# Optimization experiments

Measured on AMD Instinct MI355X. Metric: run time of the kernel, lower is better.

The kernel has to match this reference:

```python
import jax, jax.numpy as jnp
import numpy as np

B, S, D, H, HH, L = 256, 512, 128, 256, 128, 64
PATH_V, SYS_V = 10000, 500

def _gru_cell(gi_t, h, Whh, bhh):
    # PyTorch GRU cell: gi_t = x @ Wih.T + bih precomputed
    gh = h @ Whh.T + bhh
    ir, iz, inn = jnp.split(gi_t, 3, axis=-1)
    hr, hz, hn = jnp.split(gh, 3, axis=-1)
    r = jax.nn.sigmoid(ir + hr)
    z = jax.nn.sigmoid(iz + hz)
    n = jnp.tanh(inn + r * hn)
    return (1.0 - z) * n + z * h

def _gru_seq(x, Wih, Whh, bih, bhh):
    # x: [B,S,in] -> outputs [B,S,H], zero initial hidden (torch default)
    gi = jnp.einsum('bsd,hd->bsh', x, Wih) + bih  # precompute input gates once
    h0 = jnp.zeros((x.shape[0], Whh.shape[1]), x.dtype)
    def step(h, gi_t):
        hn = _gru_cell(gi_t, h, Whh, bhh)
        return hn, hn
    _, ys = jax.lax.scan(step, h0, jnp.swapaxes(gi, 0, 1))
    return jnp.swapaxes(ys, 0, 1)

def setup_inputs() -> dict:
    key = jax.random.key(0)
    ks = jax.random.split(key, 24)
    r = lambda k, shape: (jax.random.normal(k, shape, dtype=jnp.float32) * 0.05)
    inp = {
        'tokens': jax.random.randint(ks[0], (B, S, 2), 0, SYS_V, dtype=jnp.int64),
        'path_emb_w': r(ks[1], (PATH_V, D)),
        'sys_emb_w': r(ks[2], (SYS_V, D)),
        # encoder gru1: D -> H
        'e1_Wih': r(ks[3], (3 * H, D)), 'e1_Whh': r(ks[4], (3 * H, H)),
        'e1_bih': r(ks[5], (3 * H,)), 'e1_bhh': r(ks[6], (3 * H,)),
        # encoder gru2: H -> HH
        'e2_Wih': r(ks[7], (3 * HH, H)), 'e2_Whh': r(ks[8], (3 * HH, HH)),
        'e2_bih': r(ks[9], (3 * HH,)), 'e2_bhh': r(ks[10], (3 * HH,)),
        # linear1: HH -> L
        'l1_W': r(ks[11], (L, HH)), 'l1_b': r(ks[12], (L,)),
        # decoder gru1: L -> HH
        'd1_Wih': r(ks[13], (3 * HH, L)), 'd1_Whh': r(ks[14], (3 * HH, HH)),
        'd1_bih': r(ks[15], (3 * HH,)), 'd1_bhh': r(ks[16], (3 * HH,)),
        # decoder gru2: HH -> H
        'd2_Wih': r(ks[17], (3 * H, HH)), 'd2_Whh': r(ks[18], (3 * H, H)),
        'd2_bih': r(ks[19], (3 * H,)), 'd2_bhh': r(ks[20], (3 * H,)),
        # linear2: H -> D
        'l2_W': r(ks[21], (D, H)), 'l2_b': r(ks[22], (D,)),
    }
    return inp

def reference(tokens, path_emb_w, sys_emb_w,
              e1_Wih, e1_Whh, e1_bih, e1_bhh,
              e2_Wih, e2_Whh, e2_bih, e2_bhh,
              l1_W, l1_b,
              d1_Wih, d1_Whh, d1_bih, d1_bhh,
              d2_Wih, d2_Whh, d2_bih, d2_bhh,
              l2_W, l2_b):
    # embedding sum -> [B,S,D]
    emb = path_emb_w[tokens[:, :, 0]] + sys_emb_w[tokens[:, :, 1]]
    # encoder (dropout is identity at eval)
    h1_seq = _gru_seq(emb, e1_Wih, e1_Whh, e1_bih, e1_bhh)      # [B,S,H]
    h2_seq = _gru_seq(h1_seq, e2_Wih, e2_Whh, e2_bih, e2_bhh)    # [B,S,HH]
    latent = h2_seq[:, -1, :] @ l1_W.T + l1_b                    # [B,L]
    gi1 = latent @ d1_Wih.T + d1_bih                             # constant [B,3*HH]
    h10 = jnp.zeros((latent.shape[0], HH), latent.dtype)
    h20 = jnp.zeros((latent.shape[0], H), latent.dtype)
    def dec_step(carry, _):
        h1, h2 = carry
        h1 = _gru_cell(gi1, h1, d1_Whh, d1_bhh)
        gi2 = h1 @ d2_Wih.T + d2_bih
        h2 = _gru_cell(gi2, h2, d2_Whh, d2_bhh)
        out = h2 @ l2_W.T + l2_b                                 # linear2 per step
        return (h1, h2), out
    _, outs = jax.lax.scan(dec_step, (h10, h20), None, length=S)  # [S,B,D]
    recon = jnp.swapaxes(outs, 0, 1)                             # [B,S,D]
    recon_loss = jnp.mean((recon - emb) ** 2)
    return latent, recon_loss
```

## Files before the change

kernel.cpp:

```cpp
#include <hip/hip_runtime.h>
#include <cstddef>

typedef unsigned short u16;
typedef __bf16 bf16x8 __attribute__((ext_vector_type(8)));
typedef float f32x4 __attribute__((ext_vector_type(4)));
typedef unsigned short us4 __attribute__((ext_vector_type(4)));

__device__ __forceinline__ u16 f2b(float f) {
    unsigned u = __float_as_uint(f);
    u += 0x7fffu + ((u >> 16) & 1u);
    return (u16)(u >> 16);
}
__device__ __forceinline__ float b2f(u16 h) { return __uint_as_float(((unsigned)h) << 16); }

__device__ __forceinline__ f32x4 mfma16(bf16x8 a, bf16x8 b, f32x4 c) {
    return __builtin_amdgcn_mfma_f32_16x16x32_bf16(a, b, c, 0, 0, 0);
}

__device__ __forceinline__ void bar_lds() {
    asm volatile("s_waitcnt lgkmcnt(0)\n\ts_barrier" ::: "memory");
}

#define CH   64
#define NCH  8
#define MCH  (CH * 256)

struct PackSeg { const float* src; u16* dst; int K; int nfrag; };
struct PackArgs { PackSeg seg[8]; };

__global__ __launch_bounds__(64) void pack_all(PackArgs pa) {
    int f = blockIdx.x;
    int i = 0;
    while (i < 7 && f >= pa.seg[i].nfrag) { f -= pa.seg[i].nfrag; i++; }
    const float* W = pa.seg[i].src;
    u16* out = pa.seg[i].dst;
    int K = pa.seg[i].K;
    int lane = threadIdx.x, q = lane >> 4, ln = lane & 15;
    int KT = K >> 5;
    int nt = f / KT, kt = f % KT;
    int n = nt * 16 + ln;
    int kb = kt * 32 + q * 8;
#pragma unroll
    for (int j = 0; j < 8; j++)
        out[((size_t)f * 64 + lane) * 8 + j] = f2b(W[(size_t)n * K + kb + j]);
}

__global__ void zero_kernel(float* __restrict__ st, float* __restrict__ lossslot) {
    int i = blockIdx.x * 256 + threadIdx.x;
    if (i < 196608) st[i] = 0.f;
    if (i == 0) *lossslot = 0.f;
}

__global__ __launch_bounds__(256) void embed_kernel(const int* __restrict__ tok,
                                                    const float* __restrict__ pw,
                                                    const float* __restrict__ sw,
                                                    u16* __restrict__ emb) {
    int col = threadIdx.x & 127;
    int half = threadIdx.x >> 7;
    int rbase = blockIdx.x * 16;
#pragma unroll
    for (int i = 0; i < 8; i++) {
        int r = rbase + i * 2 + half;
        int b = r & 255, t = r >> 8;
        const int* tp = tok + ((size_t)b * 512 + t) * 2;
        float v = pw[(size_t)tp[0] * 128 + col] + sw[(size_t)tp[1] * 128 + col];
        emb[(size_t)r * 128 + col] = f2b(v);
    }
}

template <int K, int N>
__device__ __forceinline__ void gemm_body(int bid, char* ldsraw,
                                          const u16* __restrict__ X,
                                          const u16* __restrict__ Wp,
                                          const float* __restrict__ bias,
                                          const float* __restrict__ bhh,
                                          u16* __restrict__ out) {
    constexpr int NH = N / 2, KT = K / 32, NTL = NH / 16;
    u16* wl = (u16*)ldsraw;
    int tid = threadIdx.x, wid = tid >> 6, lane = tid & 63, q = lane >> 4, ln = lane & 15;
    int half = bid & 1, mg = bid >> 1;
    {
        const bf16x8* src = (const bf16x8*)(Wp + (size_t)half * NH * K);
        bf16x8* dst = (bf16x8*)wl;
#pragma unroll
        for (int i = 0; i < NH * K / 8 / 512; i++) dst[tid + i * 512] = src[tid + i * 512];
    }
    __syncthreads();
    int m0 = (mg * 8 + wid) * 16;
    int t = m0 >> 8, bg = (m0 >> 4) & 15;
    u16* obase = out + (size_t)(t * 16 + bg) * N * 16;
    bf16x8 af[KT];
#pragma unroll
    for (int kt = 0; kt < KT; kt++)
        af[kt] = *(const bf16x8*)(X + (size_t)(m0 + ln) * K + kt * 32 + q * 8);
    for (int nt = 0; nt < NTL; nt++) {
        f32x4 acc = {0.f, 0.f, 0.f, 0.f};
#pragma unroll
        for (int kt = 0; kt < KT; kt++)
            acc = mfma16(af[kt], *(const bf16x8*)&wl[((nt * KT + kt) * 64 + lane) * 8], acc);
        int g = half * NH + nt * 16 + ln;
        float bv = bias[g] + ((g < 2 * (N / 3)) ? bhh[g] : 0.f);
        us4 v;
#pragma unroll
        for (int r = 0; r < 4; r++) v[r] = f2b(acc[r] + bv);
        *(us4*)&obase[(size_t)g * 16 + 4 * q] = v;
    }
}

template <int K, int N>
__global__ __launch_bounds__(512, 2) void gemm_kernel(const u16* __restrict__ X,
                                                      const u16* __restrict__ Wp,
                                                      const float* __restrict__ bias,
                                                      const float* __restrict__ bhh,
                                                      u16* __restrict__ out) {
    __shared__ char lds[98304];
    gemm_body<K, N>(blockIdx.x, lds, X, Wp, bias, bhh, out);
}

__device__ __forceinline__ void loss_body(int bid, char* ldsraw,
                                          const u16* __restrict__ h2d,
                                          const u16* __restrict__ Wp,
                                          const float* __restrict__ l2b,
                                          const u16* __restrict__ embc,
                                          float* __restrict__ loss) {
    float* red = (float*)ldsraw;
    int tid = threadIdx.x, wid = tid >> 6, lane = tid & 63, q = lane >> 4, ln = lane & 15;
    int m0 = (bid * 8 + wid) * 16;
    bf16x8 af[8];
#pragma unroll
    for (int kt = 0; kt < 8; kt++)
        af[kt] = *(const bf16x8*)(h2d + (size_t)(m0 + ln) * 256 + kt * 32 + q * 8);
    float ls = 0.f;
#pragma unroll
    for (int nt = 0; nt < 8; nt++) {
        f32x4 acc = {0.f, 0.f, 0.f, 0.f};
#pragma unroll
        for (int kt = 0; kt < 8; kt++)
            acc = mfma16(af[kt], *(const bf16x8*)(Wp + ((size_t)(nt * 8 + kt) * 64 + lane) * 8), acc);
        int g = nt * 16 + ln;
        float bv = l2b[g];
#pragma unroll
        for (int r = 0; r < 4; r++) {
            float rec = acc[r] + bv;
            float ev = b2f(embc[(size_t)(m0 + q * 4 + r) * 128 + g]);
            float d = rec - ev;
            ls += d * d;
        }
    }
    red[tid] = ls;
    __syncthreads();
    for (int s = 256; s > 0; s >>= 1) {
        if (tid < s) red[tid] += red[tid + s];
        __syncthreads();
    }
    if (tid == 0) atomicAdd(loss, red[0] * (1.f / 16777216.f));
}

template <int H, bool GI_CONST, bool WRITE_SEQ>
__device__ __forceinline__ void rec_body(int bid, char* ldsraw,
                                         const u16* __restrict__ giT,
                                         const float* __restrict__ gic,
                                         const u16* __restrict__ Wp,
                                         const float* __restrict__ bhh,
                                         float* __restrict__ hstate,
                                         u16* __restrict__ hseq, int steps) {
    constexpr int G3 = 3 * H;
    constexpr int KT = H / 32;
    constexpr int NHF = H / 128;
    constexpr int HP = H + 8;
    constexpr bool WLDS = (H == 256);
    constexpr int NREG = 3 * NHF - (WLDS ? 1 : 0);

    u16* wl = (u16*)ldsraw;
    u16 (*hl)[16][HP] = (u16 (*)[16][HP])(ldsraw + (WLDS ? 65536 : 0));

    const int tid = threadIdx.x, w = tid >> 6, lane = tid & 63, q = lane >> 4, ln = lane & 15;
    const int b0 = bid * 16;
    const bf16x8* wpv = (const bf16x8*)Wp;

    bf16x8 wfr[NREG][KT];
#pragma unroll
    for (int ti = 0; ti < NREG; ti++) {
        const int g = ti / NHF, h = ti % NHF;
#pragma unroll
        for (int kt = 0; kt < KT; kt++)
            wfr[ti][kt] = wpv[((size_t)(g * (H / 16) + NHF * w + h) * KT + kt) * 64 + lane];
    }
    if (WLDS) {
#pragma unroll
        for (int kt = 0; kt < KT; kt++)
            *(bf16x8*)&wl[((w * KT + kt) * 64 + lane) * 8] =
                wpv[((size_t)(2 * (H / 16) + NHF * w + (NHF - 1)) * KT + kt) * 64 + lane];
    }
    float bhn_r[NHF];
#pragma unroll
    for (int h = 0; h < NHF; h++) bhn_r[h] = bhh[2 * H + 16 * (NHF * w + h) + ln];

    float hold[NHF][4];
#pragma unroll
    for (int h = 0; h < NHF; h++)
#pragma unroll
        for (int rg = 0; rg < 4; rg++) {
            const int b = 4 * q + rg, k = 16 * (NHF * w + h) + ln;
            u16 hb = f2b(hstate[(size_t)(b0 + b) * H + k]);
            hold[h][rg] = b2f(hb);
            hl[0][b][k] = hb;
        }

    float gcf[3][NHF][4];
    us4 gp[3][NHF];
    int loff[3][NHF];
    if (GI_CONST) {
#pragma unroll
        for (int g = 0; g < 3; g++)
#pragma unroll
            for (int h = 0; h < NHF; h++)
#pragma unroll
                for (int rg = 0; rg < 4; rg++)
                    gcf[g][h][rg] =
                        gic[(size_t)(b0 + 4 * q + rg) * G3 + g * H + 16 * (NHF * w + h) + ln];
    } else {
#pragma unroll
        for (int g = 0; g < 3; g++)
#pragma unroll
            for (int h = 0; h < NHF; h++) {
                loff[g][h] = (g * H + 16 * (NHF * w + h) + ln) * 16 + 4 * q;
                gp[g][h] = *(const us4*)&giT[(size_t)bid * G3 * 16 + loff[g][h]];
            }
    }
    bar_lds();

    for (int t = 0; t < steps; t++) {
        const int p = t & 1;
        float gf2[NHF][4];
        f32x4 acc[3][NHF];
#pragma unroll
        for (int h = 0; h < NHF; h++)
#pragma unroll
            for (int rg = 0; rg < 4; rg++) {
                if (GI_CONST) {
                    acc[0][h][rg] = gcf[0][h][rg];
                    acc[1][h][rg] = gcf[1][h][rg];
                    gf2[h][rg] = gcf[2][h][rg];
                } else {
                    acc[0][h][rg] = b2f(gp[0][h][rg]);
                    acc[1][h][rg] = b2f(gp[1][h][rg]);
                    gf2[h][rg] = b2f(gp[2][h][rg]);
                }
                acc[2][h][rg] = 0.f;
            }
        if (!GI_CONST) {
            const int tn = (t + 1 < steps) ? t + 1 : t;
            const u16* blk = giT + (size_t)(tn * 16 + bid) * G3 * 16;
#pragma unroll
            for (int g = 0; g < 3; g++)
#pragma unroll
                for (int h = 0; h < NHF; h++) gp[g][h] = *(const us4*)&blk[loff[g][h]];
        }

#pragma unroll
        for (int kh = 0; kh < KT / 2; kh++) {
            bf16x8 af0 = *(const bf16x8*)&hl[p][ln][(2 * kh) * 32 + q * 8];
            bf16x8 af1 = *(const bf16x8*)&hl[p][ln][(2 * kh + 1) * 32 + q * 8];
#pragma unroll
            for (int ti = 0; ti < NREG; ti++) {
                const int g = ti / NHF, h = ti % NHF;
                acc[g][h] = mfma16(af0, wfr[ti][2 * kh], acc[g][h]);
                acc[g][h] = mfma16(af1, wfr[ti][2 * kh + 1], acc[g][h]);
            }
            if (WLDS) {
                bf16x8 w0 = *(const bf16x8*)&wl[((w * KT + 2 * kh) * 64 + lane) * 8];
                bf16x8 w1 = *(const bf16x8*)&wl[((w * KT + 2 * kh + 1) * 64 + lane) * 8];
                acc[2][NHF - 1] = mfma16(af0, w0, acc[2][NHF - 1]);
                acc[2][NHF - 1] = mfma16(af1, w1, acc[2][NHF - 1]);
            }
        }

#pragma unroll
        for (int h = 0; h < NHF; h++)
#pragma unroll
            for (int rg = 0; rg < 4; rg++) {
                float xr = acc[0][h][rg];
                float xz = acc[1][h][rg];
                float hn = acc[2][h][rg] + bhn_r[h];
                float r = __builtin_amdgcn_rcpf(1.f + __builtin_amdgcn_exp2f(-1.44269504f * xr));
                float z = __builtin_amdgcn_rcpf(1.f + __builtin_amdgcn_exp2f(-1.44269504f * xz));
                float y = gf2[h][rg] + r * hn;
                float e2 = __builtin_amdgcn_exp2f(2.88539008f * y);
                float n = 1.f - 2.f * __builtin_amdgcn_rcpf(e2 + 1.f);
                float hv = n + z * (hold[h][rg] - n);
                u16 hb = f2b(hv);
                hold[h][rg] = b2f(hb);
                const int k = 16 * (NHF * w + h) + ln;
                hl[p ^ 1][4 * q + rg][k] = hb;
                if (WRITE_SEQ) hseq[((size_t)t * 256 + b0 + 4 * q + rg) * H + k] = hb;
            }
        bar_lds();
    }
#pragma unroll
    for (int h = 0; h < NHF; h++)
#pragma unroll
        for (int rg = 0; rg < 4; rg++)
            hstate[(size_t)(b0 + 4 * q + rg) * H + 16 * (NHF * w + h) + ln] = hold[h][rg];
}

__global__ __launch_bounds__(512, 2) void enc_pair(
    int nb1, int nb2, int ng1,
    const u16* r1gi, const u16* r1W, const float* r1bhh, float* r1st, u16* r1seq,
    const u16* r2gi, const u16* r2W, const float* r2bhh, float* r2st,
    const u16* g1X, const u16* g1W, const float* g1b, const float* g1bhh, u16* g1out,
    const u16* g2X, const u16* g2W, const float* g2b, const float* g2bhh, u16* g2out,
    int steps) {
    __shared__ char lds[98304];
    int b = blockIdx.x;
    if (b < nb1)
        rec_body<256, false, true>(b, lds, r1gi, nullptr, r1W, r1bhh, r1st, r1seq, steps);
    else if (b < nb1 + nb2)
        rec_body<128, false, false>(b - nb1, lds, r2gi, nullptr, r2W, r2bhh, r2st, nullptr, steps);
    else if (b < nb1 + nb2 + ng1)
        gemm_body<128, 768>(b - nb1 - nb2, lds, g1X, g1W, g1b, g1bhh, g1out);
    else
        gemm_body<256, 384>(b - nb1 - nb2 - ng1, lds, g2X, g2W, g2b, g2bhh, g2out);
}

__global__ __launch_bounds__(512, 2) void dec_pair(
    int nb1, int nb2, int ng,
    const float* r1gic, const u16* r1W, const float* r1bhh, float* r1st, u16* r1seq,
    const u16* r2gi, const u16* r2W, const float* r2bhh, float* r2st, u16* r2seq,
    const u16* gX, const u16* gW, const float* gb, const float* gbhh, u16* gout,
    const u16* lh2, const u16* lW, const float* l2b, const u16* lemb, float* lloss,
    int steps) {
    __shared__ char lds[98304];
    int b = blockIdx.x;
    if (b < nb1)
        rec_body<128, true, true>(b, lds, nullptr, r1gic, r1W, r1bhh, r1st, r1seq, steps);
    else if (b < nb1 + nb2)
        rec_body<256, false, true>(b - nb1, lds, r2gi, nullptr, r2W, r2bhh, r2st, r2seq, steps);
    else if (b < nb1 + nb2 + ng)
        gemm_body<128, 768>(b - nb1 - nb2, lds, gX, gW, gb, gbhh, gout);
    else
        loss_body(b - nb1 - nb2 - ng, lds, lh2, lW, l2b, lemb, lloss);
}

__global__ __launch_bounds__(128) void latent_kernel(const float* __restrict__ st2,
                                                     const float* __restrict__ l1W,
                                                     const float* __restrict__ l1b,
                                                     const float* __restrict__ d1Wih,
                                                     const float* __restrict__ d1bih,
                                                     const float* __restrict__ d1bhh,
                                                     float* __restrict__ dout,
                                                     float* __restrict__ gi1dec) {
    __shared__ float hv[128], lat[64];
    int b = blockIdx.x, tid = threadIdx.x;
    hv[tid] = st2[(size_t)b * 128 + tid];
    __syncthreads();
    if (tid < 64) {
        float s = l1b[tid];
        for (int k = 0; k < 128; k++) s += l1W[tid * 128 + k] * hv[k];
        dout[b * 64 + tid] = s;
        lat[tid] = s;
    }
    __syncthreads();
    for (int g = tid; g < 384; g += 128) {
        float s = d1bih[g] + (g < 256 ? d1bhh[g] : 0.f);
        for (int k = 0; k < 64; k++) s += d1Wih[g * 64 + k] * lat[k];
        gi1dec[(size_t)b * 384 + g] = s;
    }
}

extern "C" void kernel_launch(void* const* d_in, const int* in_sizes, int n_in,
                              void* d_out, int out_size, void* d_ws, size_t ws_size,
                              hipStream_t stream) {
    (void)in_sizes; (void)n_in; (void)out_size; (void)ws_size;
    const int*   tok   = (const int*)d_in[0];
    const float* pw    = (const float*)d_in[1];
    const float* sw    = (const float*)d_in[2];
    const float* e1Wih = (const float*)d_in[3];
    const float* e1Whh = (const float*)d_in[4];
    const float* e1bih = (const float*)d_in[5];
    const float* e1bhh = (const float*)d_in[6];
    const float* e2Wih = (const float*)d_in[7];
    const float* e2Whh = (const float*)d_in[8];
    const float* e2bih = (const float*)d_in[9];
    const float* e2bhh = (const float*)d_in[10];
    const float* l1W   = (const float*)d_in[11];
    const float* l1b   = (const float*)d_in[12];
    const float* d1Wih = (const float*)d_in[13];
    const float* d1Whh = (const float*)d_in[14];
    const float* d1bih = (const float*)d_in[15];
    const float* d1bhh = (const float*)d_in[16];
    const float* d2Wih = (const float*)d_in[17];
    const float* d2Whh = (const float*)d_in[18];
    const float* d2bih = (const float*)d_in[19];
    const float* d2bhh = (const float*)d_in[20];
    const float* l2W   = (const float*)d_in[21];
    const float* l2b   = (const float*)d_in[22];
    float* dout = (float*)d_out;

    char* base = (char*)d_ws;
    size_t o = 0;
    auto alloc = [&](size_t bytes) { size_t r = o; o += (bytes + 255) & ~(size_t)255; return r; };
    u16* e1Wih_p = (u16*)(base + alloc(196608));
    u16* e1Whh_p = (u16*)(base + alloc(393216));
    u16* e2Wih_p = (u16*)(base + alloc(196608));
    u16* e2Whh_p = (u16*)(base + alloc(98304));
    u16* d1Whh_p = (u16*)(base + alloc(98304));
    u16* d2Wih_p = (u16*)(base + alloc(196608));
    u16* d2Whh_p = (u16*)(base + alloc(393216));
    u16* l2W_p   = (u16*)(base + alloc(65536));
    u16* emb_p   = (u16*)(base + alloc((size_t)131072 * 128 * 2));
    u16* giA0    = (u16*)(base + alloc((size_t)MCH * 768 * 2));
    u16* giA1    = (u16*)(base + alloc((size_t)MCH * 768 * 2));
    u16* giB0    = (u16*)(base + alloc((size_t)MCH * 384 * 2));
    u16* giB1    = (u16*)(base + alloc((size_t)MCH * 384 * 2));
    u16* h1c0    = (u16*)(base + alloc((size_t)MCH * 256 * 2));
    u16* h1c1    = (u16*)(base + alloc((size_t)MCH * 256 * 2));
    u16* h2c0    = (u16*)(base + alloc((size_t)MCH * 256 * 2));
    u16* h2c1    = (u16*)(base + alloc((size_t)MCH * 256 * 2));
    float* st1 = (float*)(base + alloc(256 * 256 * 4));
    float* st2 = (float*)(base + alloc(256 * 128 * 4));
    float* st3 = (float*)(base + alloc(256 * 128 * 4));
    float* st4 = (float*)(base + alloc(256 * 256 * 4));
    float* gi1dec = (float*)(base + alloc(256 * 384 * 4));
    u16* giA[2] = {giA0, giA1};
    u16* giB[2] = {giB0, giB1};
    u16* h1c[2] = {h1c0, h1c1};
    u16* h2c[2] = {h2c0, h2c1};

    PackArgs pa;
    pa.seg[0] = {e1Wih, e1Wih_p, 128, 192};
    pa.seg[1] = {e1Whh, e1Whh_p, 256, 384};
    pa.seg[2] = {e2Wih, e2Wih_p, 256, 192};
    pa.seg[3] = {e2Whh, e2Whh_p, 128, 96};
    pa.seg[4] = {d1Whh, d1Whh_p, 128, 96};
    pa.seg[5] = {d2Wih, d2Wih_p, 128, 192};
    pa.seg[6] = {d2Whh, d2Whh_p, 256, 384};
    pa.seg[7] = {l2W,   l2W_p,   256, 64};
    pack_all<<<1600, 64, 0, stream>>>(pa);
    zero_kernel<<<769, 256, 0, stream>>>(st1, dout + 16384);
    embed_kernel<<<8192, 256, 0, stream>>>(tok, pw, sw, emb_p);

    gemm_kernel<128, 768><<<256, 512, 0, stream>>>(emb_p, e1Wih_p, e1bih, e1bhh, giA[0]);
    for (int c = 0; c < NCH; c++) {
        int nb2 = (c >= 2) ? 16 : 0;
        int ng1 = (c <= 6) ? 256 : 0;
        int ng2 = (c >= 1) ? 256 : 0;
        enc_pair<<<16 + nb2 + ng1 + ng2, 512, 0, stream>>>(16, nb2, ng1,
            giA[c & 1], e1Whh_p, e1bhh, st1, h1c[c & 1],
            giB[(c - 2) & 1], e2Whh_p, e2bhh, st2,
            emb_p + (size_t)((c + 1) & 7) * MCH * 128, e1Wih_p, e1bih, e1bhh, giA[(c + 1) & 1],
            h1c[(c - 1) & 1], e2Wih_p, e2bih, e2bhh, giB[(c - 1) & 1], CH);
    }
    enc_pair<<<16 + 256, 512, 0, stream>>>(0, 16, 0,
        giA[0], e1Whh_p, e1bhh, st1, h1c[0],
        giB[0], e2Whh_p, e2bhh, st2,
        emb_p, e1Wih_p, e1bih, e1bhh, giA[0],
        h1c[1], e2Wih_p, e2bih, e2bhh, giB[1], CH);
    enc_pair<<<16, 512, 0, stream>>>(0, 16, 0,
        giA[0], e1Whh_p, e1bhh, st1, h1c[0],
        giB[1], e2Whh_p, e2bhh, st2,
        emb_p, e1Wih_p, e1bih, e1bhh, giA[0],
        h1c[0], e2Wih_p, e2bih, e2bhh, giB[0], CH);

    latent_kernel<<<256, 128, 0, stream>>>(st2, l1W, l1b, d1Wih, d1bih, d1bhh, dout, gi1dec);

    for (int c = 0; c <= 10; c++) {
        int nb1 = (c <= 7) ? 16 : 0;
        int ng  = (c >= 1 && c <= 8) ? 256 : 0;
        int nb2 = (c >= 2 && c <= 9) ? 16 : 0;
        int nl  = (c >= 3) ? 128 : 0;
        dec_pair<<<nb1 + nb2 + ng + nl, 512, 0, stream>>>(nb1, nb2, ng,
            gi1dec, d1Whh_p, d1bhh, st3, h1c[c & 1],
            giA[(c - 2) & 1], d2Whh_p, d2bhh, st4, h2c[(c - 2) & 1],
            h1c[(c - 1) & 1], d2Wih_p, d2bih, d2bhh, giA[(c - 1) & 1],
            h2c[(c - 3) & 1], l2W_p, l2b, emb_p + (size_t)((c - 3) & 7) * MCH * 128,
            dout + 16384, CH);
    }
}
```

Measured before the change: 1.917 ms.

## Halve workgroup size so each wave owns twice the GRU tiles

All fused kernels now launch with 256 threads (4 waves) instead of 512. In the recurrent body each wave holds twice as many hidden-unit tiles of the recurrent weights in registers, and the LDS weight and hidden-state regions are resized to match. In the GEMM and loss bodies each wave loops over two row tiles. The aim is a cheaper per-step barrier and one wave per SIMD in the latency-bound recurrence. The cost is much higher VGPR pressure, which the launch bounds now allow, and fewer resident waves for the overlapped GEMM blocks.

```diff
diff --git a/kernel.cpp b/kernel.cpp
--- a/kernel.cpp
+++ b/kernel.cpp
@@ -83,32 +83,35 @@
         const bf16x8* src = (const bf16x8*)(Wp + (size_t)half * NH * K);
         bf16x8* dst = (bf16x8*)wl;
 #pragma unroll
-        for (int i = 0; i < NH * K / 8 / 512; i++) dst[tid + i * 512] = src[tid + i * 512];
+        for (int i = 0; i < NH * K / 8 / 256; i++) dst[tid + i * 256] = src[tid + i * 256];
     }
     __syncthreads();
-    int m0 = (mg * 8 + wid) * 16;
-    int t = m0 >> 8, bg = (m0 >> 4) & 15;
-    u16* obase = out + (size_t)(t * 16 + bg) * N * 16;
-    bf16x8 af[KT];
-#pragma unroll
-    for (int kt = 0; kt < KT; kt++)
-        af[kt] = *(const bf16x8*)(X + (size_t)(m0 + ln) * K + kt * 32 + q * 8);
-    for (int nt = 0; nt < NTL; nt++) {
-        f32x4 acc = {0.f, 0.f, 0.f, 0.f};
+#pragma unroll
+    for (int tt = 0; tt < 2; tt++) {
+        int m0 = (mg * 8 + tt * 4 + wid) * 16;
+        int t = m0 >> 8, bg = (m0 >> 4) & 15;
+        u16* obase = out + (size_t)(t * 16 + bg) * N * 16;
+        bf16x8 af[KT];
 #pragma unroll
         for (int kt = 0; kt < KT; kt++)
-            acc = mfma16(af[kt], *(const bf16x8*)&wl[((nt * KT + kt) * 64 + lane) * 8], acc);
-        int g = half * NH + nt * 16 + ln;
-        float bv = bias[g] + ((g < 2 * (N / 3)) ? bhh[g] : 0.f);
-        us4 v;
-#pragma unroll
-        for (int r = 0; r < 4; r++) v[r] = f2b(acc[r] + bv);
-        *(us4*)&obase[(size_t)g * 16 + 4 * q] = v;
+            af[kt] = *(const bf16x8*)(X + (size_t)(m0 + ln) * K + kt * 32 + q * 8);
+        for (int nt = 0; nt < NTL; nt++) {
+            f32x4 acc = {0.f, 0.f, 0.f, 0.f};
+#pragma unroll
+            for (int kt = 0; kt < KT; kt++)
+                acc = mfma16(af[kt], *(const bf16x8*)&wl[((nt * KT + kt) * 64 + lane) * 8], acc);
+            int g = half * NH + nt * 16 + ln;
+            float bv = bias[g] + ((g < 2 * (N / 3)) ? bhh[g] : 0.f);
+            us4 v;
+#pragma unroll
+            for (int r = 0; r < 4; r++) v[r] = f2b(acc[r] + bv);
+            *(us4*)&obase[(size_t)g * 16 + 4 * q] = v;
+        }
     }
 }
 
 template <int K, int N>
-__global__ __launch_bounds__(512, 2) void gemm_kernel(const u16* __restrict__ X,
+__global__ __launch_bounds__(256, 1) void gemm_kernel(const u16* __restrict__ X,
                                                       const u16* __restrict__ Wp,
                                                       const float* __restrict__ bias,
                                                       const float* __restrict__ bhh,
@@ -125,31 +128,34 @@
                                           float* __restrict__ loss) {
     float* red = (float*)ldsraw;
     int tid = threadIdx.x, wid = tid >> 6, lane = tid & 63, q = lane >> 4, ln = lane & 15;
-    int m0 = (bid * 8 + wid) * 16;
-    bf16x8 af[8];
-#pragma unroll
-    for (int kt = 0; kt < 8; kt++)
-        af[kt] = *(const bf16x8*)(h2d + (size_t)(m0 + ln) * 256 + kt * 32 + q * 8);
     float ls = 0.f;
 #pragma unroll
-    for (int nt = 0; nt < 8; nt++) {
-        f32x4 acc = {0.f, 0.f, 0.f, 0.f};
+    for (int tt = 0; tt < 2; tt++) {
+        int m0 = (bid * 8 + tt * 4 + wid) * 16;
+        bf16x8 af[8];
 #pragma unroll
         for (int kt = 0; kt < 8; kt++)
-            acc = mfma16(af[kt], *(const bf16x8*)(Wp + ((size_t)(nt * 8 + kt) * 64 + lane) * 8), acc);
-        int g = nt * 16 + ln;
-        float bv = l2b[g];
-#pragma unroll
-        for (int r = 0; r < 4; r++) {
-            float rec = acc[r] + bv;
-            float ev = b2f(embc[(size_t)(m0 + q * 4 + r) * 128 + g]);
-            float d = rec - ev;
-            ls += d * d;
+            af[kt] = *(const bf16x8*)(h2d + (size_t)(m0 + ln) * 256 + kt * 32 + q * 8);
+#pragma unroll
+        for (int nt = 0; nt < 8; nt++) {
+            f32x4 acc = {0.f, 0.f, 0.f, 0.f};
+#pragma unroll
+            for (int kt = 0; kt < 8; kt++)
+                acc = mfma16(af[kt], *(const bf16x8*)(Wp + ((size_t)(nt * 8 + kt) * 64 + lane) * 8), acc);
+            int g = nt * 16 + ln;
+            float bv = l2b[g];
+#pragma unroll
+            for (int r = 0; r < 4; r++) {
+                float rec = acc[r] + bv;
+                float ev = b2f(embc[(size_t)(m0 + q * 4 + r) * 128 + g]);
+                float d = rec - ev;
+                ls += d * d;
+            }
         }
     }
     red[tid] = ls;
     __syncthreads();
-    for (int s = 256; s > 0; s >>= 1) {
+    for (int s = 128; s > 0; s >>= 1) {
         if (tid < s) red[tid] += red[tid + s];
         __syncthreads();
     }
@@ -166,13 +172,13 @@
                                          u16* __restrict__ hseq, int steps) {
     constexpr int G3 = 3 * H;
     constexpr int KT = H / 32;
-    constexpr int NHF = H / 128;
+    constexpr int THW = (H / 16) / 4;
     constexpr int HP = H + 8;
     constexpr bool WLDS = (H == 256);
-    constexpr int NREG = 3 * NHF - (WLDS ? 1 : 0);
+    constexpr int NREG = 3 * THW - (WLDS ? 1 : 0);
 
     u16* wl = (u16*)ldsraw;
-    u16 (*hl)[16][HP] = (u16 (*)[16][HP])(ldsraw + (WLDS ? 65536 : 0));
+    u16 (*hl)[16][HP] = (u16 (*)[16][HP])(ldsraw + (WLDS ? 32768 : 0));
 
     const int tid = threadIdx.x, w = tid >> 6, lane = tid & 63, q = lane >> 4, ln = lane & 15;
     const int b0 = bid * 16;
@@ -181,73 +187,71 @@
     bf16x8 wfr[NREG][KT];
 #pragma unroll
     for (int ti = 0; ti < NREG; ti++) {
-        const int g = ti / NHF, h = ti % NHF;
+        const int g = ti / THW, hh = ti % THW;
 #pragma unroll
         for (int kt = 0; kt < KT; kt++)
-            wfr[ti][kt] = wpv[((size_t)(g * (H / 16) + NHF * w + h) * KT + kt) * 64 + lane];
+            wfr[ti][kt] = wpv[((size_t)(g * (H / 16) + THW * w + hh) * KT + kt) * 64 + lane];
     }
     if (WLDS) {
 #pragma unroll
         for (int kt = 0; kt < KT; kt++)
             *(bf16x8*)&wl[((w * KT + kt) * 64 + lane) * 8] =
-                wpv[((size_t)(2 * (H / 16) + NHF * w + (NHF - 1)) * KT + kt) * 64 + lane];
-    }
-    float bhn_r[NHF];
-#pragma unroll
-    for (int h = 0; h < NHF; h++) bhn_r[h] = bhh[2 * H + 16 * (NHF * w + h) + ln];
-
-    float hold[NHF][4];
-#pragma unroll
-    for (int h = 0; h < NHF; h++)
+                wpv[((size_t)(2 * (H / 16) + THW * w + (THW - 1)) * KT + kt) * 64 + lane];
+    }
+    float bhn_r[THW];
+#pragma unroll
+    for (int hh = 0; hh < THW; hh++) bhn_r[hh] = bhh[2 * H + 16 * (THW * w + hh) + ln];
+
+    float hold[THW][4];
+#pragma unroll
+    for (int hh = 0; hh < THW; hh++)
 #pragma unroll
         for (int rg = 0; rg < 4; rg++) {
-            const int b = 4 * q + rg, k = 16 * (NHF * w + h) + ln;
+            const int b = 4 * q + rg, k = 16 * (THW * w + hh) + ln;
             u16 hb = f2b(hstate[(size_t)(b0 + b) * H + k]);
-            hold[h][rg] = b2f(hb);
+            hold[hh][rg] = b2f(hb);
             hl[0][b][k] = hb;
         }
 
-    float gcf[3][NHF][4];
-    us4 gp[3][NHF];
-    int loff[3][NHF];
+    float gcf[3][THW][4];
+    us4 gp[3][THW];
     if (GI_CONST) {
 #pragma unroll
         for (int g = 0; g < 3; g++)
 #pragma unroll
-            for (int h = 0; h < NHF; h++)
+            for (int hh = 0; hh < THW; hh++)
 #pragma unroll
                 for (int rg = 0; rg < 4; rg++)
-                    gcf[g][h][rg] =
-                        gic[(size_t)(b0 + 4 * q + rg) * G3 + g * H + 16 * (NHF * w + h) + ln];
+                    gcf[g][hh][rg] =
+                        gic[(size_t)(b0 + 4 * q + rg) * G3 + g * H + 16 * (THW * w + hh) + ln];
     } else {
+        const u16* blk = giT + (size_t)bid * G3 * 16;
 #pragma unroll
         for (int g = 0; g < 3; g++)
 #pragma unroll
-            for (int h = 0; h < NHF; h++) {
-                loff[g][h] = (g * H + 16 * (NHF * w + h) + ln) * 16 + 4 * q;
-                gp[g][h] = *(const us4*)&giT[(size_t)bid * G3 * 16 + loff[g][h]];
-            }
+            for (int hh = 0; hh < THW; hh++)
+                gp[g][hh] = *(const us4*)&blk[(g * H + 16 * (THW * w + hh) + ln) * 16 + 4 * q];
     }
     bar_lds();
 
     for (int t = 0; t < steps; t++) {
         const int p = t & 1;
-        float gf2[NHF][4];
-        f32x4 acc[3][NHF];
-#pragma unroll
-        for (int h = 0; h < NHF; h++)
+        float gf2[THW][4];
+        f32x4 acc[3][THW];
+#pragma unroll
+        for (int hh = 0; hh < THW; hh++)
 #pragma unroll
             for (int rg = 0; rg < 4; rg++) {
                 if (GI_CONST) {
-                    acc[0][h][rg] = gcf[0][h][rg];
-                    acc[1][h][rg] = gcf[1][h][rg];
-                    gf2[h][rg] = gcf[2][h][rg];
+                    acc[0][hh][rg] = gcf[0][hh][rg];
+                    acc[1][hh][rg] = gcf[1][hh][rg];
+                    gf2[hh][rg] = gcf[2][hh][rg];
                 } else {
-                    acc[0][h][rg] = b2f(gp[0][h][rg]);
-                    acc[1][h][rg] = b2f(gp[1][h][rg]);
-                    gf2[h][rg] = b2f(gp[2][h][rg]);
+                    acc[0][hh][rg] = b2f(gp[0][hh][rg]);
+                    acc[1][hh][rg] = b2f(gp[1][hh][rg]);
+                    gf2[hh][rg] = b2f(gp[2][hh][rg]);
                 }
-                acc[2][h][rg] = 0.f;
+                acc[2][hh][rg] = 0.f;
             }
         if (!GI_CONST) {
             const int tn = (t + 1 < steps) ? t + 1 : t;
@@ -255,7 +259,8 @@
 #pragma unroll
             for (int g = 0; g < 3; g++)
 #pragma unroll
-                for (int h = 0; h < NHF; h++) gp[g][h] = *(const us4*)&blk[loff[g][h]];
+                for (int hh = 0; hh < THW; hh++)
+                    gp[g][hh] = *(const us4*)&blk[(g * H + 16 * (THW * w + hh) + ln) * 16 + 4 * q];
         }
 
 #pragma unroll
@@ -264,47 +269,47 @@
             bf16x8 af1 = *(const bf16x8*)&hl[p][ln][(2 * kh + 1) * 32 + q * 8];
 #pragma unroll
             for (int ti = 0; ti < NREG; ti++) {
-                const int g = ti / NHF, h = ti % NHF;
-                acc[g][h] = mfma16(af0, wfr[ti][2 * kh], acc[g][h]);
-                acc[g][h] = mfma16(af1, wfr[ti][2 * kh + 1], acc[g][h]);
+                const int g = ti / THW, hh = ti % THW;
+                acc[g][hh] = mfma16(af0, wfr[ti][2 * kh], acc[g][hh]);
+                acc[g][hh] = mfma16(af1, wfr[ti][2 * kh + 1], acc[g][hh]);
             }
             if (WLDS) {
                 bf16x8 w0 = *(const bf16x8*)&wl[((w * KT + 2 * kh) * 64 + lane) * 8];
                 bf16x8 w1 = *(const bf16x8*)&wl[((w * KT + 2 * kh + 1) * 64 + lane) * 8];
-                acc[2][NHF - 1] = mfma16(af0, w0, acc[2][NHF - 1]);
-                acc[2][NHF - 1] = mfma16(af1, w1, acc[2][NHF - 1]);
+                acc[2][THW - 1] = mfma16(af0, w0, acc[2][THW - 1]);
+                acc[2][THW - 1] = mfma16(af1, w1, acc[2][THW - 1]);
             }
         }
 
 #pragma unroll
-        for (int h = 0; h < NHF; h++)
+        for (int hh = 0; hh < THW; hh++)
 #pragma unroll
             for (int rg = 0; rg < 4; rg++) {
-                float xr = acc[0][h][rg];
-                float xz = acc[1][h][rg];
-                float hn = acc[2][h][rg] + bhn_r[h];
+                float xr = acc[0][hh][rg];
+                float xz = acc[1][hh][rg];
+                float hn = acc[2][hh][rg] + bhn_r[hh];
                 float r = __builtin_amdgcn_rcpf(1.f + __builtin_amdgcn_exp2f(-1.44269504f * xr));
                 float z = __builtin_amdgcn_rcpf(1.f + __builtin_amdgcn_exp2f(-1.44269504f * xz));
-                float y = gf2[h][rg] + r * hn;
+                float y = gf2[hh][rg] + r * hn;
                 float e2 = __builtin_amdgcn_exp2f(2.88539008f * y);
                 float n = 1.f - 2.f * __builtin_amdgcn_rcpf(e2 + 1.f);
-                float hv = n + z * (hold[h][rg] - n);
+                float hv = n + z * (hold[hh][rg] - n);
                 u16 hb = f2b(hv);
-                hold[h][rg] = b2f(hb);
-                const int k = 16 * (NHF * w + h) + ln;
+                hold[hh][rg] = b2f(hb);
+                const int k = 16 * (THW * w + hh) + ln;
                 hl[p ^ 1][4 * q + rg][k] = hb;
                 if (WRITE_SEQ) hseq[((size_t)t * 256 + b0 + 4 * q + rg) * H + k] = hb;
             }
         bar_lds();
     }
 #pragma unroll
-    for (int h = 0; h < NHF; h++)
+    for (int hh = 0; hh < THW; hh++)
 #pragma unroll
         for (int rg = 0; rg < 4; rg++)
-            hstate[(size_t)(b0 + 4 * q + rg) * H + 16 * (NHF * w + h) + ln] = hold[h][rg];
-}
-
-__global__ __launch_bounds__(512, 2) void enc_pair(
+            hstate[(size_t)(b0 + 4 * q + rg) * H + 16 * (THW * w + hh) + ln] = hold[hh][rg];
+}
+
+__global__ __launch_bounds__(256, 1) void enc_pair(
     int nb1, int nb2, int ng1,
     const u16* r1gi, const u16* r1W, const float* r1bhh, float* r1st, u16* r1seq,
     const u16* r2gi, const u16* r2W, const float* r2bhh, float* r2st,
@@ -323,7 +328,7 @@
         gemm_body<256, 384>(b - nb1 - nb2 - ng1, lds, g2X, g2W, g2b, g2bhh, g2out);
 }
 
-__global__ __launch_bounds__(512, 2) void dec_pair(
+__global__ __launch_bounds__(256, 1) void dec_pair(
     int nb1, int nb2, int ng,
     const float* r1gic, const u16* r1W, const float* r1bhh, float* r1st, u16* r1seq,
     const u16* r2gi, const u16* r2W, const float* r2bhh, float* r2st, u16* r2seq,
@@ -440,23 +445,23 @@
     zero_kernel<<<769, 256, 0, stream>>>(st1, dout + 16384);
     embed_kernel<<<8192, 256, 0, stream>>>(tok, pw, sw, emb_p);
 
-    gemm_kernel<128, 768><<<256, 512, 0, stream>>>(emb_p, e1Wih_p, e1bih, e1bhh, giA[0]);
+    gemm_kernel<128, 768><<<256, 256, 0, stream>>>(emb_p, e1Wih_p, e1bih, e1bhh, giA[0]);
     for (int c = 0; c < NCH; c++) {
         int nb2 = (c >= 2) ? 16 : 0;
         int ng1 = (c <= 6) ? 256 : 0;
         int ng2 = (c >= 1) ? 256 : 0;
-        enc_pair<<<16 + nb2 + ng1 + ng2, 512, 0, stream>>>(16, nb2, ng1,
+        enc_pair<<<16 + nb2 + ng1 + ng2, 256, 0, stream>>>(16, nb2, ng1,
             giA[c & 1], e1Whh_p, e1bhh, st1, h1c[c & 1],
             giB[(c - 2) & 1], e2Whh_p, e2bhh, st2,
             emb_p + (size_t)((c + 1) & 7) * MCH * 128, e1Wih_p, e1bih, e1bhh, giA[(c + 1) & 1],
             h1c[(c - 1) & 1], e2Wih_p, e2bih, e2bhh, giB[(c - 1) & 1], CH);
     }
-    enc_pair<<<16 + 256, 512, 0, stream>>>(0, 16, 0,
+    enc_pair<<<16 + 256, 256, 0, stream>>>(0, 16, 0,
         giA[0], e1Whh_p, e1bhh, st1, h1c[0],
         giB[0], e2Whh_p, e2bhh, st2,
         emb_p, e1Wih_p, e1bih, e1bhh, giA[0],
         h1c[1], e2Wih_p, e2bih, e2bhh, giB[1], CH);
-    enc_pair<<<16, 512, 0, stream>>>(0, 16, 0,
+    enc_pair<<<16, 256, 0, stream>>>(0, 16, 0,
         giA[0], e1Whh_p, e1bhh, st1, h1c[0],
         giB[1], e2Whh_p, e2bhh, st2,
         emb_p, e1Wih_p, e1bih, e1bhh, giA[0],
@@ -469,7 +474,7 @@
         int ng  = (c >= 1 && c <= 8) ? 256 : 0;
         int nb2 = (c >= 2 && c <= 9) ? 16 : 0;
         int nl  = (c >= 3) ? 128 : 0;
-        dec_pair<<<nb1 + nb2 + ng + nl, 512, 0, stream>>>(nb1, nb2, ng,
+        dec_pair<<<nb1 + nb2 + ng + nl, 256, 0, stream>>>(nb1, nb2, ng,
             gi1dec, d1Whh_p, d1bhh, st3, h1c[c & 1],
             giA[(c - 2) & 1], d2Whh_p, d2bhh, st4, h2c[(c - 2) & 1],
             h1c[(c - 1) & 1], d2Wih_p, d2bih, d2bhh, giA[(c - 1) & 1],
```

After: 2.837 ms. 48.0% more time.
